# Performance work log

Measured on AMD Instinct MI355X. Metric: run time of the kernel, lower is better.

The kernel has to match this reference:

```python
import jax, jax.numpy as jnp
import numpy as np


def setup_inputs() -> dict:
    key = jax.random.key(0)
    ks = jax.random.split(key, 6)
    N, D, H, C = 4096, 2048, 512, 200
    feats = jax.random.normal(ks[0], (N, D), dtype=jnp.float32)
    targets = jax.random.randint(ks[1], (N,), 0, C)
    w1 = jax.random.normal(ks[2], (2 * D, H), dtype=jnp.float32) * 0.02
    b1 = jnp.zeros((H,), dtype=jnp.float32)
    w2 = jax.random.normal(ks[3], (H, D), dtype=jnp.float32) * 0.02
    b2 = jnp.zeros((D,), dtype=jnp.float32)
    wfc = jax.random.normal(ks[4], (D, C), dtype=jnp.float32) * 0.02
    bfc = jnp.zeros((C,), dtype=jnp.float32)
    return {"feats": feats, "targets": targets, "w1": w1, "b1": b1,
            "w2": w2, "b2": b2, "wfc": wfc, "bfc": bfc}


def _match_pair(feats, targets):
    # pairwise Euclidean distances (N x N)
    sq = jnp.sum(feats * feats, axis=1)
    d2 = sq[:, None] + sq[None, :] - 2.0 * (feats @ feats.T)
    dist = jnp.sqrt(jnp.maximum(d2, 0.0))
    same = targets[:, None] == targets[None, :]
    inf = jnp.asarray(jnp.inf, dist.dtype)
    # nearest same-class neighbor, skipping self (distance 0 is rank 0)
    m_intra = jnp.where(same, dist, inf)
    intras = jnp.argsort(m_intra, axis=1)[:, 1]
    # nearest different-class neighbor
    m_inter = jnp.where(same, inf, dist)
    inters = jnp.argmin(m_inter, axis=1)
    return feats[intras], feats[inters], targets[inters]


def reference(feats, targets, w1, b1, w2, b2, wfc, bfc):
    intra_feats, inter_feats, inter_labels = _match_pair(feats, targets)
    x_feat = jnp.concatenate([feats, feats], axis=0)           # 2N x D
    y_feat = jnp.concatenate([intra_feats, inter_feats], axis=0)
    # MLP (dropout inactive at eval)
    h = jnp.concatenate([x_feat, y_feat], axis=1) @ w1 + b1
    m_feat = h @ w2 + b2
    gate_x = jax.nn.sigmoid(m_feat * x_feat)
    gate_y = jax.nn.sigmoid(m_feat * y_feat)
    x_self = x_feat + x_feat * gate_x
    x_other = x_feat + x_feat * gate_y
    y_self = y_feat + y_feat * gate_y
    y_other = y_feat + y_feat * gate_x
    logit1_self = jax.nn.sigmoid(x_self @ wfc + bfc)
    logit1_other = jax.nn.sigmoid(x_other @ wfc + bfc)
    logit2_self = jax.nn.sigmoid(y_self @ wfc + bfc)
    logit2_other = jax.nn.sigmoid(y_other @ wfc + bfc)
    labels1 = jnp.concatenate([targets, targets], axis=0)
    labels2 = jnp.concatenate([targets, inter_labels], axis=0)
    return (logit1_self, logit1_other, logit2_self, logit2_other, labels1, labels2)
```

## Files before the change

kernel.cpp:

```cpp
#include <hip/hip_runtime.h>
#include <math.h>

#define N 4096
#define D 2048
#define H 512
#define C 200
#define NR 8192
#define LDH 40

typedef unsigned long long u64;
typedef unsigned int u32;
typedef float f32x4 __attribute__((ext_vector_type(4)));
typedef _Float16 f16x8 __attribute__((ext_vector_type(8)));
typedef _Float16 f16x4 __attribute__((ext_vector_type(4)));

__device__ __forceinline__ float sigm(float z) { return 1.0f / (1.0f + expf(-z)); }
__device__ __forceinline__ float bf2f(unsigned short u) { return __uint_as_float(((u32)u) << 16); }
__device__ __forceinline__ unsigned short f2bf(float x) {
  u32 u = __float_as_uint(x);
  return (unsigned short)((u + 0x7fffu + ((u >> 16) & 1u)) >> 16);
}

__device__ __forceinline__ void gll16(const _Float16* g, _Float16* l) {
  __builtin_amdgcn_global_load_lds(
      (const __attribute__((address_space(1))) u32*)g,
      (__attribute__((address_space(3))) u32*)l, 16, 0, 0);
}

__global__ __launch_bounds__(256) void kc_pack_k1(const float* __restrict__ f,
                                                  _Float16* __restrict__ hiP,
                                                  _Float16* __restrict__ loP,
                                                  float* __restrict__ sq,
                                                  u64* __restrict__ bi,
                                                  u64* __restrict__ be) {
  __shared__ float wsum[4];
  const int r = blockIdx.x;
  const int t = threadIdx.x;
  const int kb = t >> 2, slot = t & 3;
  const float* src = f + (size_t)r * D + t * 8;
  float4 v0 = *(const float4*)src;
  float4 v1 = *(const float4*)(src + 4);
  f16x8 hv, lv;
  const float xs[8] = {v0.x, v0.y, v0.z, v0.w, v1.x, v1.y, v1.z, v1.w};
  float s = 0.0f;
#pragma unroll
  for (int j = 0; j < 8; ++j) {
    const _Float16 h = (_Float16)xs[j];
    hv[j] = h;
    lv[j] = (_Float16)(xs[j] - (float)h);
    s += xs[j] * xs[j];
  }
  const size_t off = ((size_t)((r >> 7) * 64 + kb) * 128 + (r & 127)) * 32 +
                     ((slot ^ ((r >> 1) & 3)) << 3);
  *(f16x8*)(hiP + off) = hv;
  *(f16x8*)(loP + off) = lv;
  for (int o = 32; o > 0; o >>= 1) s += __shfl_down(s, o);
  if ((t & 63) == 0) wsum[t >> 6] = s;
  __syncthreads();
  if (t == 0) {
    sq[r] = wsum[0] + wsum[1] + wsum[2] + wsum[3];
    bi[r] = ~0ull; be[r] = ~0ull;
  }
}

__global__ void kc_T(const float* __restrict__ in, _Float16* __restrict__ out,
                     int R, int Cc) {
  __shared__ float t[32][33];
  const int c0 = blockIdx.x * 32, r0 = blockIdx.y * 32;
  for (int i = threadIdx.y; i < 32; i += 8)
    t[i][threadIdx.x] = in[(size_t)(r0 + i) * Cc + c0 + threadIdx.x];
  __syncthreads();
  for (int i = threadIdx.y; i < 32; i += 8)
    out[(size_t)(c0 + i) * R + r0 + threadIdx.x] = (_Float16)t[threadIdx.x][i];
}

__global__ __launch_bounds__(256) void kc_packW(const float* __restrict__ w,
                                                _Float16* __restrict__ wP,
                                                int Ncols, int KB) {
  __shared__ float t[32][132];
  const int tid = threadIdx.x;
  const int kb = blockIdx.x, nb = blockIdx.y;
#pragma unroll
  for (int it = 0; it < 4; ++it) {
    const int idx = it * 256 + tid;
    const int k = idx >> 5, nq = idx & 31;
    float4 v = *(const float4*)(w + (size_t)(kb * 32 + k) * Ncols + nb * 128 + nq * 4);
    t[k][nq * 4 + 0] = v.x; t[k][nq * 4 + 1] = v.y;
    t[k][nq * 4 + 2] = v.z; t[k][nq * 4 + 3] = v.w;
  }
  __syncthreads();
#pragma unroll
  for (int it = 0; it < 2; ++it) {
    const int idx = it * 256 + tid;
    const int n = idx >> 2, slot = idx & 3;
    f16x8 v;
#pragma unroll
    for (int j = 0; j < 8; ++j) v[j] = (_Float16)t[slot * 8 + j][n];
    *(f16x8*)(wP + ((size_t)(nb * KB + kb) * 128 + n) * 32 +
              ((slot ^ ((n >> 1) & 3)) << 3)) = v;
  }
}

__global__ __launch_bounds__(64) void kc_wfc(const float* __restrict__ wfc,
                                             _Float16* __restrict__ wfcP) {
  const int kc = blockIdx.x, nf = blockIdx.y, l = threadIdx.x;
  const int n = nf * 16 + (l & 15);
  const int k = kc * 32 + (l >> 4) * 8;
  f16x8 v;
#pragma unroll
  for (int j = 0; j < 8; ++j)
    v[j] = (n < C) ? (_Float16)wfc[(size_t)(k + j) * C + n] : (_Float16)0.0f;
  *(f16x8*)(wfcP + ((size_t)(kc * 14 + nf) * 64 + l) * 8) = v;
}

__global__ __launch_bounds__(256, 2) void k2_dist(
    const _Float16* __restrict__ fhiP, const _Float16* __restrict__ floP,
    const int* __restrict__ tgt, const float* __restrict__ sq,
    u64* __restrict__ bi, u64* __restrict__ be) {
  __shared__ __align__(16) _Float16 S[4][4096];
  __shared__ float sqi[128], sqj[128];
  __shared__ int ti[128], tj[128];
  __shared__ u64 Li[2][128], Lj[2][128];

  const int tid = threadIdx.x;
  const int bid = blockIdx.x;
  const int b = (bid & 7) * 66 + (bid >> 3);
  int bj = (int)((sqrtf(8.0f * (float)b + 1.0f) - 1.0f) * 0.5f);
  while ((bj + 1) * (bj + 2) / 2 <= b) ++bj;
  while (bj * (bj + 1) / 2 > b) --bj;
  const int bib = b - bj * (bj + 1) / 2;
  const int i0 = bib * 128, j0 = bj * 128;
  const bool diag = (i0 == j0);

  const int l = tid & 63;
  const int w = tid >> 6;
  const int wr = w >> 1, wc = w & 1;
  const int fr = l & 15, fg = l >> 4;
  const int pswz = ((fr >> 1) & 3) << 3;

  const _Float16* psrc = ((w & 1) ? floP : fhiP) +
                         ((size_t)((w < 2 ? bib : bj) * 64) * 4096) + l * 8;

  if (tid < 128) { sqi[tid] = sq[i0 + tid]; ti[tid] = tgt[i0 + tid]; }
  else { const int t = tid - 128; sqj[t] = sq[j0 + t]; tj[t] = tgt[j0 + t]; }
  ((u64*)Li)[tid] = ~0ull;
  ((u64*)Lj)[tid] = ~0ull;

  f32x4 acc[4][4] = {};

  for (int k = 0; k < 64; ++k) {
    {
      const _Float16* gsrc = psrc + (size_t)k * 4096;
      _Float16* ldst = &S[w][0];
#pragma unroll
      for (int ii = 0; ii < 8; ++ii) gll16(gsrc + ii * 512, ldst + ii * 512);
    }
    __syncthreads();
    f16x8 ah[4], al[4], bh[4], bl[4];
#pragma unroll
    for (int m = 0; m < 4; ++m) {
      const int off = (wr * 64 + m * 16 + fr) * 32 + ((fg << 3) ^ pswz);
      ah[m] = *(const f16x8*)&S[0][off];
      al[m] = *(const f16x8*)&S[1][off];
    }
#pragma unroll
    for (int n = 0; n < 4; ++n) {
      const int off = (wc * 64 + n * 16 + fr) * 32 + ((fg << 3) ^ pswz);
      bh[n] = *(const f16x8*)&S[2][off];
      bl[n] = *(const f16x8*)&S[3][off];
    }
#pragma unroll
    for (int m = 0; m < 4; ++m)
#pragma unroll
      for (int n = 0; n < 4; ++n) {
        acc[m][n] = __builtin_amdgcn_mfma_f32_16x16x32_f16(ah[m], bh[n], acc[m][n], 0, 0, 0);
        acc[m][n] = __builtin_amdgcn_mfma_f32_16x16x32_f16(ah[m], bl[n], acc[m][n], 0, 0, 0);
        acc[m][n] = __builtin_amdgcn_mfma_f32_16x16x32_f16(al[m], bh[n], acc[m][n], 0, 0, 0);
      }
    __syncthreads();
  }

#pragma unroll
  for (int m = 0; m < 4; ++m) {
#pragma unroll
    for (int reg = 0; reg < 4; ++reg) {
      const int row_l = wr * 64 + m * 16 + fg * 4 + reg;
      const float si = sqi[row_l];
      const int ci = ti[row_l];
      u64 ks = ~0ull, kd = ~0ull;
#pragma unroll
      for (int n = 0; n < 4; ++n) {
        const int col_l = wc * 64 + n * 16 + fr;
        const float d2 = si + sqj[col_l] - 2.0f * acc[m][n][reg];
        const u64 key = ((u64)__float_as_uint(d2) << 32) | (u32)(j0 + col_l);
        if (ci == tj[col_l]) {
          if (i0 + row_l != j0 + col_l) ks = key < ks ? key : ks;
        } else {
          kd = key < kd ? key : kd;
        }
      }
#pragma unroll
      for (int off = 1; off < 16; off <<= 1) {
        u64 o = __shfl_xor(ks, off); ks = o < ks ? o : ks;
        o = __shfl_xor(kd, off);     kd = o < kd ? o : kd;
      }
      if (fr == 0) {
        if (ks != ~0ull) atomicMin(&Li[0][row_l], ks);
        if (kd != ~0ull) atomicMin(&Li[1][row_l], kd);
      }
    }
  }
  if (!diag) {
#pragma unroll
    for (int n = 0; n < 4; ++n) {
      const int col_l = wc * 64 + n * 16 + fr;
      const float sj = sqj[col_l];
      const int cj = tj[col_l];
      u64 ks = ~0ull, kd = ~0ull;
#pragma unroll
      for (int m = 0; m < 4; ++m)
#pragma unroll
        for (int reg = 0; reg < 4; ++reg) {
          const int row_l = wr * 64 + m * 16 + fg * 4 + reg;
          const float d2 = sqi[row_l] + sj - 2.0f * acc[m][n][reg];
          const u64 key = ((u64)__float_as_uint(d2) << 32) | (u32)(i0 + row_l);
          if (ti[row_l] == cj) ks = key < ks ? key : ks;
          else                 kd = key < kd ? key : kd;
        }
#pragma unroll
      for (int off = 16; off < 64; off <<= 1) {
        u64 o = __shfl_xor(ks, off); ks = o < ks ? o : ks;
        o = __shfl_xor(kd, off);     kd = o < kd ? o : kd;
      }
      if (fg == 0) {
        if (ks != ~0ull) atomicMin(&Lj[0][col_l], ks);
        if (kd != ~0ull) atomicMin(&Lj[1][col_l], kd);
      }
    }
  }
  __syncthreads();
  if (tid < 128) {
    u64 v = Li[0][tid]; if (v != ~0ull) atomicMin(&bi[i0 + tid], v);
    v = Li[1][tid];     if (v != ~0ull) atomicMin(&be[i0 + tid], v);
  } else if (!diag) {
    const int t = tid - 128;
    u64 v = Lj[0][t]; if (v != ~0ull) atomicMin(&bi[j0 + t], v);
    v = Lj[1][t];     if (v != ~0ull) atomicMin(&be[j0 + t], v);
  }
}

__global__ __launch_bounds__(256) void k3_prep(const int* __restrict__ tgt,
                                               const u64* __restrict__ bi,
                                               const u64* __restrict__ be,
                                               int* __restrict__ iy,
                                               float* __restrict__ lab1,
                                               float* __restrict__ lab2) {
  const int r = blockIdx.x * 256 + threadIdx.x;
  if (r >= NR) return;
  if (r < N) {
    iy[r] = (int)(bi[r] & 0xffffffffull);
    const float t = (float)tgt[r];
    lab1[r] = t; lab2[r] = t;
  } else {
    const int s = r - N;
    const int j = (int)(be[s] & 0xffffffffull);
    iy[r] = j;
    lab1[r] = (float)tgt[s];
    lab2[r] = (float)tgt[j];
  }
}

__global__ __launch_bounds__(256, 4) void k4_h(const _Float16* __restrict__ fhiP,
                                               const _Float16* __restrict__ w1P,
                                               const float* __restrict__ b1,
                                               const int* __restrict__ iy,
                                               _Float16* __restrict__ hout) {
  __shared__ __align__(16) _Float16 As[2 * 2048];
  __shared__ __align__(16) _Float16 Bs[2 * 4096];
  __shared__ int iy_s[64];
  const int tid = threadIdx.x;
  const int bid = blockIdx.x;
  const int b = (bid & 7) * 64 + (bid >> 3);
  const int nIdx = b >> 7, mIdx = b & 127;
  const int r0 = mIdx * 64, n0 = nIdx * 128;
  if (tid < 64) iy_s[tid] = iy[r0 + tid];
  const int l = tid & 63, w = tid >> 6;
  const int fr = l & 15, fg = l >> 4;
  const int pswz = ((fr >> 1) & 3) << 3;
  f32x4 acc[4][2] = {};
  const int gr0 = r0 & (N - 1);
  const _Float16* paBase = fhiP + ((size_t)((gr0 >> 7) * 64) * 4096) + (gr0 & 127) * 32;

#define K4_MFMA()                                                                   \
  do {                                                                              \
    _Pragma("unroll") for (int p = 0; p < 2; ++p) {                                 \
      f16x8 a[4], bb[2];                                                            \
      _Pragma("unroll") for (int m = 0; m < 4; ++m)                                 \
        a[m] = *(const f16x8*)&As[p * 2048 + (m * 16 + fr) * 32 + ((fg << 3) ^ pswz)]; \
      _Pragma("unroll") for (int nf = 0; nf < 2; ++nf)                              \
        bb[nf] = *(const f16x8*)&Bs[p * 4096 + (w * 32 + nf * 16 + fr) * 32 +       \
                                    ((fg << 3) ^ pswz)];                            \
      _Pragma("unroll") for (int m = 0; m < 4; ++m)                                 \
        _Pragma("unroll") for (int nf = 0; nf < 2; ++nf)                            \
          acc[m][nf] = __builtin_amdgcn_mfma_f32_16x16x32_f16(a[m], bb[nf],         \
                                                              acc[m][nf], 0, 0, 0); \
    }                                                                               \
  } while (0)

  for (int ks = 0; ks < 32; ++ks) {
    const int kbA = ks * 2;
    __syncthreads();
    {
      const _Float16* pa = paBase + (size_t)kbA * 4096 + l * 8;
      const _Float16* pb = w1P + (size_t)(nIdx * 128 + kbA) * 4096 + l * 8;
#pragma unroll
      for (int cc = 0; cc < 6; ++cc) {
        const int c = w * 6 + cc;
        if (c < 8) {
          const int p = c >> 2, co = c & 3;
          gll16(pa + p * 4096 + co * 512, &As[p * 2048 + co * 512]);
        } else {
          const int cb = c - 8;
          gll16(pb + cb * 512, &Bs[cb * 512]);
        }
      }
    }
    __syncthreads();
    K4_MFMA();
  }
  for (int ks = 0; ks < 32; ++ks) {
    const int kbA = ks * 2;
    const int kbW = 64 + ks * 2;
    __syncthreads();
    {
      const _Float16* pb = w1P + (size_t)(nIdx * 128 + kbW) * 4096 + l * 8;
#pragma unroll
      for (int cc = 0; cc < 4; ++cc) {
        const int cb = w * 4 + cc;
        gll16(pb + cb * 512, &Bs[cb * 512]);
      }
    }
#pragma unroll
    for (int it = 0; it < 2; ++it) {
      const int idx = it * 256 + tid;
      const int row = idx >> 3, p = (idx >> 2) & 1, slot = idx & 3;
      const int gy = iy_s[row];
      const _Float16* src = fhiP +
          ((size_t)((gy >> 7) * 64 + kbA + p) * 128 + (gy & 127)) * 32 +
          ((slot ^ ((gy >> 1) & 3)) << 3);
      *(uint4*)&As[p * 2048 + row * 32 + ((slot ^ ((row >> 1) & 3)) << 3)] =
          *(const uint4*)src;
    }
    __syncthreads();
    K4_MFMA();
  }
#undef K4_MFMA

#pragma unroll
  for (int nf = 0; nf < 2; ++nf) {
    const int gcol = n0 + w * 32 + nf * 16 + fr;
    const float bias = b1[gcol];
#pragma unroll
    for (int m = 0; m < 4; ++m)
#pragma unroll
      for (int reg = 0; reg < 4; ++reg) {
        const int grow = r0 + m * 16 + fg * 4 + reg;
        hout[(size_t)grow * H + gcol] = (_Float16)(acc[m][nf][reg] + bias);
      }
  }
}

__global__ __launch_bounds__(256, 2) void k5_m(const _Float16* __restrict__ hbuf,
                                               const _Float16* __restrict__ w2T,
                                               const float* __restrict__ b2,
                                               unsigned short* __restrict__ mbuf) {
  __shared__ __align__(16) _Float16 As[128 * LDH], Bs[128 * LDH];
  const int tid = threadIdx.x;
  const int bid = blockIdx.x;
  const int b = (bid & 7) * 128 + (bid >> 3);
  const int n0 = (b & 15) * 128, r0 = (b >> 4) * 128;
  const int l = tid & 63, w = tid >> 6;
  const int wr = w >> 1, wc = w & 1, fr = l & 15, fg = l >> 4;
  f32x4 acc[4][4] = {};

  for (int k0 = 0; k0 < H; k0 += 32) {
    __syncthreads();
#pragma unroll
    for (int it = 0; it < 2; ++it) {
      const int c = it * 256 + tid;
      const int row = c >> 2, xc = c & 3;
      const int la = row * LDH + xc * 8;
      *(uint4*)&As[la] = *(const uint4*)(hbuf + (size_t)(r0 + row) * H + k0 + xc * 8);
      *(uint4*)&Bs[la] = *(const uint4*)(w2T + (size_t)(n0 + row) * H + k0 + xc * 8);
    }
    __syncthreads();
    f16x8 a[4], bb[4];
#pragma unroll
    for (int m = 0; m < 4; ++m) a[m] = *(const f16x8*)&As[(wr * 64 + m * 16 + fr) * LDH + fg * 8];
#pragma unroll
    for (int n = 0; n < 4; ++n) bb[n] = *(const f16x8*)&Bs[(wc * 64 + n * 16 + fr) * LDH + fg * 8];
#pragma unroll
    for (int m = 0; m < 4; ++m)
#pragma unroll
      for (int n = 0; n < 4; ++n)
        acc[m][n] = __builtin_amdgcn_mfma_f32_16x16x32_f16(a[m], bb[n], acc[m][n], 0, 0, 0);
  }
#pragma unroll
  for (int n = 0; n < 4; ++n) {
    const int gcol = n0 + wc * 64 + n * 16 + fr;
    const float bias = b2[gcol];
#pragma unroll
    for (int m = 0; m < 4; ++m)
#pragma unroll
      for (int reg = 0; reg < 4; ++reg) {
        const int grow = r0 + wr * 64 + m * 16 + fg * 4 + reg;
        mbuf[(size_t)grow * D + gcol] = f2bf(acc[m][n][reg] + bias);
      }
  }
}

__global__ __launch_bounds__(256, 2) void k6_logits(
    const float* __restrict__ feats, const unsigned short* __restrict__ mbuf,
    const int* __restrict__ iy, const _Float16* __restrict__ wfcP,
    const float* __restrict__ bfc, float* __restrict__ out) {
  __shared__ __align__(16) _Float16 As[64 * 64];
  __shared__ int iy_s[16];
  const int tid = threadIdx.x;
  const int r0 = blockIdx.x * 16;
  const int l = tid & 63, v = tid >> 6;
  const int fr = l & 15, fg = l >> 4;
  if (tid < 16) iy_s[tid] = iy[r0 + tid];
  __syncthreads();
  const int rr = tid >> 4;
  const int kq = (tid & 15) << 2;
  const int rg = r0 + rr;
  const float* xptr = feats + (size_t)(rg & (N - 1)) * D;
  const float* yptr = feats + (size_t)iy_s[rr] * D;
  const unsigned short* mptr = mbuf + (size_t)rg * D;
  const int wsw = ((rr >> 1) & 3) | ((rr & 1) << 2);
  const int soff = ((((kq >> 3) ^ wsw)) << 3) + (kq & 7);
  const int rsw = (((fr >> 1) & 3) | ((fr & 1) << 2)) << 3;

  f32x4 acc[14] = {};
  float4 xv = *(const float4*)(xptr + kq);
  float4 yv = *(const float4*)(yptr + kq);
  ushort4 mv = *(const ushort4*)(mptr + kq);

  for (int k0 = 0; k0 < D; k0 += 64) {
    __syncthreads();
    {
      const float xs[4] = {xv.x, xv.y, xv.z, xv.w};
      const float ys[4] = {yv.x, yv.y, yv.z, yv.w};
      const unsigned short ms[4] = {mv.x, mv.y, mv.z, mv.w};
      f16x4 a0, a1, a2, a3;
#pragma unroll
      for (int j = 0; j < 4; ++j) {
        const float x = xs[j], y = ys[j], m = bf2f(ms[j]);
        const float gx = sigm(m * x), gy = sigm(m * y);
        a0[j] = (_Float16)(x * (1.0f + gx));
        a1[j] = (_Float16)(x * (1.0f + gy));
        a2[j] = (_Float16)(y * (1.0f + gy));
        a3[j] = (_Float16)(y * (1.0f + gx));
      }
      *(f16x4*)&As[(rr)      * 64 + soff] = a0;
      *(f16x4*)&As[(16 + rr) * 64 + soff] = a1;
      *(f16x4*)&As[(32 + rr) * 64 + soff] = a2;
      *(f16x4*)&As[(48 + rr) * 64 + soff] = a3;
    }
    if (k0 + 64 < D) {
      xv = *(const float4*)(xptr + k0 + 64 + kq);
      yv = *(const float4*)(yptr + k0 + 64 + kq);
      mv = *(const ushort4*)(mptr + k0 + 64 + kq);
    }
    __syncthreads();
#pragma unroll
    for (int ksl = 0; ksl < 2; ++ksl) {
      const f16x8 af =
          *(const f16x8*)&As[(v * 16 + fr) * 64 + ((((ksl * 4 + fg) << 3)) ^ rsw)];
      const _Float16* bp = wfcP + (size_t)((k0 >> 5) + ksl) * 14 * 512 + (size_t)l * 8;
#pragma unroll
      for (int nf = 0; nf < 14; ++nf) {
        const f16x8 bf = *(const f16x8*)(bp + nf * 512);
        acc[nf] = __builtin_amdgcn_mfma_f32_16x16x32_f16(af, bf, acc[nf], 0, 0, 0);
      }
    }
  }
  float* outv = out + (size_t)v * NR * C;
#pragma unroll
  for (int nf = 0; nf < 14; ++nf) {
    const int col = nf * 16 + fr;
    if (col < C) {
      const float bias = bfc[col];
#pragma unroll
      for (int reg = 0; reg < 4; ++reg) {
        const int row = r0 + fg * 4 + reg;
        outv[(size_t)row * C + col] = sigm(acc[nf][reg] + bias);
      }
    }
  }
}

extern "C" void kernel_launch(void* const* d_in, const int* in_sizes, int n_in,
                              void* d_out, int out_size, void* d_ws, size_t ws_size,
                              hipStream_t stream) {
  const float* feats = (const float*)d_in[0];
  const int*   tgt   = (const int*)d_in[1];
  const float* w1    = (const float*)d_in[2];
  const float* b1    = (const float*)d_in[3];
  const float* w2    = (const float*)d_in[4];
  const float* b2    = (const float*)d_in[5];
  const float* wfc   = (const float*)d_in[6];
  const float* bfc   = (const float*)d_in[7];
  float* out = (float*)d_out;

  char* ws = (char*)d_ws;
  float* sq = (float*)(ws);
  u64*   bi = (u64*)(ws + 16384);
  u64*   be = (u64*)(ws + 49152);
  int*   iy = (int*)(ws + 81920);
  _Float16* fhiP = (_Float16*)(ws + 131072);
  _Float16* floP = (_Float16*)(ws + 131072 + 16777216);
  unsigned short* mbuf = (unsigned short*)(ws + 131072);
  _Float16* w1P = (_Float16*)(ws + 33685504);
  _Float16* w2T = (_Float16*)(ws + 37879808);
  _Float16* hbuf = (_Float16*)(ws + 39976960);
  _Float16* wfcP = (_Float16*)(ws + 48365568);

  float* lab1 = out + (size_t)4 * NR * C;
  float* lab2 = lab1 + NR;

  kc_pack_k1<<<N, 256, 0, stream>>>(feats, fhiP, floP, sq, bi, be);
  kc_packW<<<dim3(128, 4), 256, 0, stream>>>(w1, w1P, 512, 128);
  kc_T<<<dim3(2048 / 32, 512 / 32), dim3(32, 8), 0, stream>>>(w2, w2T, 512, 2048);
  kc_wfc<<<dim3(64, 14), 64, 0, stream>>>(wfc, wfcP);
  k2_dist<<<528, 256, 0, stream>>>(fhiP, floP, tgt, sq, bi, be);
  k3_prep<<<NR / 256, 256, 0, stream>>>(tgt, bi, be, iy, lab1, lab2);
  k4_h<<<512, 256, 0, stream>>>(fhiP, w1P, b1, iy, hbuf);
  k5_m<<<1024, 256, 0, stream>>>(hbuf, w2T, b2, mbuf);
  k6_logits<<<NR / 16, 256, 0, stream>>>(feats, mbuf, iy, wfcP, bfc, out);
}
```

Measured before the change: 358.6 us.

## Double-buffer gated A tile and stage wfc B tile in LDS for logits kernel

```diff
diff --git a/kernel.cpp b/kernel.cpp
--- a/kernel.cpp
+++ b/kernel.cpp
@@ -14,7 +14,9 @@
 typedef _Float16 f16x8 __attribute__((ext_vector_type(8)));
 typedef _Float16 f16x4 __attribute__((ext_vector_type(4)));
 
-__device__ __forceinline__ float sigm(float z) { return 1.0f / (1.0f + expf(-z)); }
+__device__ __forceinline__ float sigm(float z) {
+  return __builtin_amdgcn_rcpf(1.0f + __expf(-z));
+}
 __device__ __forceinline__ float bf2f(unsigned short u) { return __uint_as_float(((u32)u) << 16); }
 __device__ __forceinline__ unsigned short f2bf(float x) {
   u32 u = __float_as_uint(x);
@@ -423,7 +425,8 @@
     const float* __restrict__ feats, const unsigned short* __restrict__ mbuf,
     const int* __restrict__ iy, const _Float16* __restrict__ wfcP,
     const float* __restrict__ bfc, float* __restrict__ out) {
-  __shared__ __align__(16) _Float16 As[64 * 64];
+  __shared__ __align__(16) _Float16 As[2][64 * 64];
+  __shared__ __align__(16) _Float16 Bs[2][14336];
   __shared__ int iy_s[16];
   const int tid = threadIdx.x;
   const int r0 = blockIdx.x * 16;
@@ -442,49 +445,69 @@
   const int rsw = (((fr >> 1) & 3) | ((fr & 1) << 2)) << 3;
 
   f32x4 acc[14] = {};
-  float4 xv = *(const float4*)(xptr + kq);
-  float4 yv = *(const float4*)(yptr + kq);
-  ushort4 mv = *(const ushort4*)(mptr + kq);
+
+#define K6_GATES(buf, xv, yv, mv)                                     \
+  do {                                                                \
+    const float xs_[4] = {xv.x, xv.y, xv.z, xv.w};                    \
+    const float ys_[4] = {yv.x, yv.y, yv.z, yv.w};                    \
+    const unsigned short ms_[4] = {mv.x, mv.y, mv.z, mv.w};           \
+    f16x4 a0, a1, a2, a3;                                             \
+    _Pragma("unroll") for (int j = 0; j < 4; ++j) {                   \
+      const float x = xs_[j], y = ys_[j], m = bf2f(ms_[j]);           \
+      const float gx = sigm(m * x), gy = sigm(m * y);                 \
+      a0[j] = (_Float16)(x * (1.0f + gx));                            \
+      a1[j] = (_Float16)(x * (1.0f + gy));                            \
+      a2[j] = (_Float16)(y * (1.0f + gy));                            \
+      a3[j] = (_Float16)(y * (1.0f + gx));                            \
+    }                                                                 \
+    *(f16x4*)&As[buf][(rr)*64 + soff] = a0;                           \
+    *(f16x4*)&As[buf][(16 + rr) * 64 + soff] = a1;                    \
+    *(f16x4*)&As[buf][(32 + rr) * 64 + soff] = a2;                    \
+    *(f16x4*)&As[buf][(48 + rr) * 64 + soff] = a3;                    \
+  } while (0)
+
+#define K6_STAGEB(k0n, buf)                                           \
+  do {                                                                \
+    const _Float16* src_ = wfcP + (size_t)((k0n) >> 5) * 7168;        \
+    _Pragma("unroll") for (int c = 0; c < 7; ++c)                     \
+      gll16(src_ + (c * 256 + tid) * 8, &Bs[buf][(c * 256 + tid) * 8]); \
+  } while (0)
+
+  {
+    float4 xv = *(const float4*)(xptr + kq);
+    float4 yv = *(const float4*)(yptr + kq);
+    ushort4 mv = *(const ushort4*)(mptr + kq);
+    K6_STAGEB(0, 0);
+    K6_GATES(0, xv, yv, mv);
+  }
 
   for (int k0 = 0; k0 < D; k0 += 64) {
-    __syncthreads();
-    {
-      const float xs[4] = {xv.x, xv.y, xv.z, xv.w};
-      const float ys[4] = {yv.x, yv.y, yv.z, yv.w};
-      const unsigned short ms[4] = {mv.x, mv.y, mv.z, mv.w};
-      f16x4 a0, a1, a2, a3;
-#pragma unroll
-      for (int j = 0; j < 4; ++j) {
-        const float x = xs[j], y = ys[j], m = bf2f(ms[j]);
-        const float gx = sigm(m * x), gy = sigm(m * y);
-        a0[j] = (_Float16)(x * (1.0f + gx));
-        a1[j] = (_Float16)(x * (1.0f + gy));
-        a2[j] = (_Float16)(y * (1.0f + gy));
-        a3[j] = (_Float16)(y * (1.0f + gx));
-      }
-      *(f16x4*)&As[(rr)      * 64 + soff] = a0;
-      *(f16x4*)&As[(16 + rr) * 64 + soff] = a1;
-      *(f16x4*)&As[(32 + rr) * 64 + soff] = a2;
-      *(f16x4*)&As[(48 + rr) * 64 + soff] = a3;
-    }
-    if (k0 + 64 < D) {
+    const int cur = (k0 >> 6) & 1;
+    __syncthreads();
+    float4 xv, yv; ushort4 mv;
+    const bool more = (k0 + 64 < D);
+    if (more) {
       xv = *(const float4*)(xptr + k0 + 64 + kq);
       yv = *(const float4*)(yptr + k0 + 64 + kq);
       mv = *(const ushort4*)(mptr + k0 + 64 + kq);
-    }
-    __syncthreads();
+      K6_STAGEB(k0 + 64, cur ^ 1);
+    }
 #pragma unroll
     for (int ksl = 0; ksl < 2; ++ksl) {
       const f16x8 af =
-          *(const f16x8*)&As[(v * 16 + fr) * 64 + ((((ksl * 4 + fg) << 3)) ^ rsw)];
-      const _Float16* bp = wfcP + (size_t)((k0 >> 5) + ksl) * 14 * 512 + (size_t)l * 8;
+          *(const f16x8*)&As[cur][(v * 16 + fr) * 64 + ((((ksl * 4 + fg) << 3)) ^ rsw)];
+      const _Float16* bp = &Bs[cur][(size_t)ksl * 7168 + (size_t)l * 8];
 #pragma unroll
       for (int nf = 0; nf < 14; ++nf) {
         const f16x8 bf = *(const f16x8*)(bp + nf * 512);
         acc[nf] = __builtin_amdgcn_mfma_f32_16x16x32_f16(af, bf, acc[nf], 0, 0, 0);
       }
     }
-  }
+    if (more) K6_GATES(cur ^ 1, xv, yv, mv);
+  }
+#undef K6_GATES
+#undef K6_STAGEB
+
   float* outv = out + (size_t)v * NR * C;
 #pragma unroll
   for (int nf = 0; nf < 14; ++nf) {
```

Measured after the change: 295.0 us, median of 2. 17.8% less time.
